# Kernel tuning notes

Hardware: AMD Instinct MI355X
Metric: run time of the kernel (lower is better)

## Reference

```python
import jax, jax.numpy as jnp
import numpy as np
from jax import lax

LB, UB = 0.0, 0.1
N_ITERS = 32  # fixed-point iterations for water-filling rebalance


def _conv(x, w, b):
    y = lax.conv_general_dilated(x, w, (1, 1), ((1, 1), (1, 1)),
                                 dimension_numbers=("NCHW", "OIHW", "NCHW"))
    return y + b[None, :, None, None]


def _maxpool2(x):
    return lax.reduce_window(x, -jnp.inf, lax.max, (1, 1, 2, 2), (1, 1, 2, 2), "VALID")


def _linear(x, w, b):
    return x @ w.T + b


def _gru(x_num, W_ih, W_hh, b_ih, b_hh):
    # x_num: [B, S, N]; torch GRU gate order r, z, n
    B = x_num.shape[0]
    H = W_hh.shape[1]
    xs = jnp.swapaxes(x_num, 0, 1)  # [S, B, N]

    def step(h, x_t):
        gi = x_t @ W_ih.T + b_ih            # [B, 3H]
        gh = h @ W_hh.T + b_hh              # [B, 3H]
        i_r, i_z, i_n = jnp.split(gi, 3, axis=-1)
        h_r, h_z, h_n = jnp.split(gh, 3, axis=-1)
        r = jax.nn.sigmoid(i_r + h_r)
        z = jax.nn.sigmoid(i_z + h_z)
        n = jnp.tanh(i_n + r * h_n)
        h_new = (1.0 - z) * n + z * h
        return h_new, None

    h0 = jnp.zeros((B, H), dtype=x_num.dtype)
    h_last, _ = lax.scan(step, h0, xs)
    return h_last


def _rebalance_one(w):
    # vectorized fixed-point version of the per-sample while-loop water-filling
    def body(carry, _):
        old, wc = carry
        leftover = jnp.sum(old - wc)
        mask = wc != UB
        s = jnp.sum(jnp.where(mask, wc, 0.0))
        gift = jnp.where(mask & (s > 0), leftover * wc / jnp.where(s > 0, s, 1.0), 0.0)
        new_old = wc + gift
        new_wc = jnp.clip(new_old, LB, UB)
        return (new_old, new_wc), None

    init = (w, jnp.clip(w, LB, UB))
    (_, wc), _ = lax.scan(body, init, None, length=N_ITERS)
    return wc


def setup_inputs() -> dict:
    key = jax.random.key(0)
    ks = jax.random.split(key, 16)
    B, S, N, H_IMG, W_IMG, HID = 16, 60, 50, 64, 60, 128
    fc_in = 64 * (H_IMG // 4) * (W_IMG // 4)  # 15360
    sc = 0.05
    return {
        "x_num": jax.random.normal(ks[0], (B, S, N), jnp.float32),
        "x_img": jax.random.uniform(ks[1], (B, N, H_IMG, W_IMG), jnp.float32),
        "conv1_w": jax.random.normal(ks[2], (32, 1, 3, 3), jnp.float32) * sc,
        "conv1_b": jnp.zeros((32,), jnp.float32),
        "conv2_w": jax.random.normal(ks[3], (64, 32, 3, 3), jnp.float32) * sc,
        "conv2_b": jnp.zeros((64,), jnp.float32),
        "fc1_w": jax.random.normal(ks[4], (64, fc_in), jnp.float32) * 0.01,
        "fc1_b": jnp.zeros((64,), jnp.float32),
        "fc_binary_w": jax.random.normal(ks[5], (1, 64), jnp.float32) * sc,
        "fc_binary_b": jnp.zeros((1,), jnp.float32),
        "fc2_w": jax.random.normal(ks[6], (128, 64), jnp.float32) * sc,
        "fc2_b": jnp.zeros((128,), jnp.float32),
        "W_ih": jax.random.normal(ks[7], (3 * HID, N), jnp.float32) * sc,
        "W_hh": jax.random.normal(ks[8], (3 * HID, HID), jnp.float32) * sc,
        "b_ih": jnp.zeros((3 * HID,), jnp.float32),
        "b_hh": jnp.zeros((3 * HID,), jnp.float32),
        "gru_fc_w": jax.random.normal(ks[9], (N, HID), jnp.float32) * sc,
        "gru_fc_b": jnp.zeros((N,), jnp.float32),
        "fusion_w": jax.random.normal(ks[10], (64, N + 128), jnp.float32) * sc,
        "fusion_b": jnp.zeros((64,), jnp.float32),
        "final_w": jax.random.normal(ks[11], (N, 64), jnp.float32) * sc,
        "final_b": jnp.zeros((N,), jnp.float32),
    }


def reference(x_num, x_img, conv1_w, conv1_b, conv2_w, conv2_b, fc1_w, fc1_b,
              fc_binary_w, fc_binary_b, fc2_w, fc2_b, W_ih, W_hh, b_ih, b_hh,
              gru_fc_w, gru_fc_b, fusion_w, fusion_b, final_w, final_b):
    B, S, N = x_num.shape
    # GRU branch: last hidden -> Linear -> [B, N]
    h_last = _gru(x_num, W_ih, W_hh, b_ih, b_hh)
    numerical_features = _linear(h_last, gru_fc_w, gru_fc_b)

    # CNN branch on per-stock chart images
    xi = x_img.reshape(B * N, 1, x_img.shape[2], x_img.shape[3])
    h = _maxpool2(jax.nn.relu(_conv(xi, conv1_w, conv1_b)))
    h = _maxpool2(jax.nn.relu(_conv(h, conv2_w, conv2_b)))
    h = h.reshape(B * N, -1)
    feats = jax.nn.relu(_linear(h, fc1_w, fc1_b))
    binary_pred = jax.nn.sigmoid(_linear(feats, fc_binary_w, fc_binary_b))
    cnn_features = _linear(feats, fc2_w, fc2_b).reshape(B, N, -1).mean(axis=1)

    fused = jax.nn.relu(_linear(jnp.concatenate([numerical_features, cnn_features], axis=1), fusion_w, fusion_b))
    w = jax.nn.softmax(_linear(fused, final_w, final_b), axis=1)
    portfolio_weights = jax.vmap(_rebalance_one)(w)
    return portfolio_weights, binary_pred.reshape(B, N)
```

## Files before the change

kernel.cpp:

```cpp
#include <hip/hip_runtime.h>
#include <hip/hip_bf16.h>

typedef unsigned short ushort_t;
typedef short short8_t __attribute__((ext_vector_type(8)));
typedef float f32x4 __attribute__((ext_vector_type(4)));
typedef float f32x16 __attribute__((ext_vector_type(16)));
typedef ushort_t us4_t __attribute__((ext_vector_type(4)));

#define NBATCH 16
#define SEQ    60
#define NSTK   50
#define HID    128
#define G3     384
#define NIMG   800
#define IH     64
#define IW     60
#define P1H    32
#define P1W    30
#define P2C    64
#define FCIN   15360

#define OFF_WIHT   0u
#define OFF_WHHF   19200u
#define OFF_WPREP  43776u
#define OFF_FC2WT  52992u
#define OFF_WFC1   61184u
#define OFF_GI     552704u
#define OFF_HLAST  921344u
#define OFF_POOL2  923392u
#define OFF_FC1P   7313152u
#define OFF_FC2O   8165120u
#define WS_FLOATS  8267520u

struct __align__(16) ConvS {
    float    imgp[66][62];
    ushort_t pool1t[34][4][34][8];
    ushort_t pool2s[64][240];
    float    w1[288];
    float    b1[32];
};
struct __align__(16) GruS {
    float    gh[16 * 388];
    ushort_t hb[16 * 136];
};
#define SMEM_BYTES 122368
#define ZWORDS ((16368 + 73984) / 4)

__device__ __forceinline__ float fast_sig(float x) {
    const float e = __expf(-x);
    return __builtin_amdgcn_rcpf(1.f + e);
}
__device__ __forceinline__ float fast_tanh(float x) {
    const float xc = fmaxf(fminf(x, 15.f), -15.f);
    const float e = __expf(2.f * xc);
    return (e - 1.f) * __builtin_amdgcn_rcpf(e + 1.f);
}

__global__ __launch_bounds__(256) void k_prep(const float* __restrict__ wih,
                                              const float* __restrict__ whh,
                                              const float* __restrict__ c2w,
                                              const float* __restrict__ fc2w,
                                              const float* __restrict__ fc1w,
                                              float* __restrict__ wihT,
                                              ushort_t* __restrict__ whhf,
                                              ushort_t* __restrict__ wprep,
                                              float* __restrict__ fc2wT,
                                              ushort_t* __restrict__ wfc1)
{
    const int idx = blockIdx.x * 256 + threadIdx.x;
    if (idx < 19200) {
        const int j = idx % G3, k = idx / G3;
        wihT[idx] = wih[j * NSTK + k];
    } else if (idx < 68352) {
        const int e = idx - 19200;
        const int i = e & 7, l = (e >> 3) & 63, ksj = e >> 9;
        const int ks = ksj & 3, jt = ksj >> 2;
        const int j = jt * 16 + (l & 15);
        const int k = ks * 32 + ((l >> 4) << 3) + i;
        __hip_bfloat16 hv = __float2bfloat16(whh[j * HID + k]);
        whhf[e] = *(ushort_t*)&hv;
    } else if (idx < 86784) {
        const int e = idx - 68352;
        const int i = e & 7, l = (e >> 3) & 63, rest = e >> 9;
        const int ks = rest & 1, mt = rest >> 1;
        const int tap = mt % 9, mm = mt / 9;
        const int oc = mm * 32 + (l & 31);
        const int ic = ks * 16 + ((l >> 5) << 3) + i;
        __hip_bfloat16 hv = __float2bfloat16(c2w[((size_t)oc * 32 + ic) * 9 + tap]);
        wprep[e] = *(ushort_t*)&hv;
    } else if (idx < 94976) {
        const int e = idx - 86784;
        const int j = e & 127, k = e >> 7;
        fc2wT[e] = fc2w[j * 64 + k];
    } else if (idx < 1078016) {
        const int e = idx - 94976;
        const int i = e & 7, l = (e >> 3) & 63, rest = e >> 9;
        const int n = rest & 3, T = rest >> 2;
        const int oc = n * 16 + (l & 15);
        const int k = T * 32 + ((l >> 4) << 3) + i;
        __hip_bfloat16 hv = __float2bfloat16(fc1w[(size_t)oc * FCIN + k]);
        wfc1[e] = *(ushort_t*)&hv;
    }
}

__global__ __launch_bounds__(384) void k_gi(const float* __restrict__ xnum,
                                            const float* __restrict__ wihT,
                                            const float* __restrict__ bih,
                                            float* __restrict__ GI)
{
    const int sb = blockIdx.x;
    const int s = sb >> 4, b = sb & 15;
    const int j = threadIdx.x;
    const float* xr = xnum + (size_t)(b * SEQ + s) * NSTK;
    float a = bih[j];
    for (int k = 0; k < NSTK; ++k) a = fmaf(xr[k], wihT[k * G3 + j], a);
    GI[((size_t)s * 16 + b) * G3 + j] = a;
}

__global__ __launch_bounds__(512, 2) void k_mega(const float* __restrict__ x_img,
                                                 const float* __restrict__ c1w,
                                                 const float* __restrict__ c1b,
                                                 const float* __restrict__ c2b,
                                                 const ushort_t* __restrict__ wprep,
                                                 const float* __restrict__ GI,
                                                 const ushort_t* __restrict__ whhf,
                                                 const float* __restrict__ bhh,
                                                 ushort_t* __restrict__ pool2,
                                                 float* __restrict__ hlast)
{
    extern __shared__ char smraw[];
    const int tid = threadIdx.x;
    const int bid = blockIdx.x;

    if (bid == 0) {
        GruS* g = (GruS*)smraw;
        const int w = tid >> 6, l = tid & 63;
        const int arow = l & 15, kq = l >> 4;
        short8_t wfr[3][4];
        #pragma unroll
        for (int jj = 0; jj < 3; ++jj)
            #pragma unroll
            for (int ks = 0; ks < 4; ++ks)
                wfr[jj][ks] = *(const short8_t*)&whhf[((((w * 3 + jj) * 4 + ks) * 64 + l) * 8)];

        const int b = tid >> 5, hh0 = (tid & 31) * 4;
        const f32x4 bhr = *(const f32x4*)&bhh[hh0];
        const f32x4 bhz = *(const f32x4*)&bhh[128 + hh0];
        const f32x4 bhn = *(const f32x4*)&bhh[256 + hh0];
        float h0 = 0.f, h1 = 0.f, h2 = 0.f, h3 = 0.f;
        for (int i = tid; i < 1088; i += 512) ((unsigned int*)g->hb)[i] = 0u;
        const float* gi0 = GI + b * G3 + hh0;
        f32x4 cr = *(const f32x4*)(gi0);
        f32x4 cz = *(const f32x4*)(gi0 + 128);
        f32x4 cn = *(const f32x4*)(gi0 + 256);
        __syncthreads();

        for (int s = 0; s < SEQ; ++s) {
            const int sn = (s + 1 < SEQ) ? s + 1 : s;
            const float* gnx = GI + ((size_t)sn * 16 + b) * G3 + hh0;
            const f32x4 nr = *(const f32x4*)(gnx);
            const f32x4 nz = *(const f32x4*)(gnx + 128);
            const f32x4 nn = *(const f32x4*)(gnx + 256);

            #pragma unroll
            for (int jj = 0; jj < 3; ++jj) {
                f32x4 a = {0.f, 0.f, 0.f, 0.f};
                #pragma unroll
                for (int ks = 0; ks < 4; ++ks) {
                    short8_t af = *(const short8_t*)&g->hb[arow * 136 + ks * 32 + kq * 8];
                    a = __builtin_amdgcn_mfma_f32_16x16x32_bf16(af, wfr[jj][ks], a, 0, 0, 0);
                }
                const int jt = w * 3 + jj;
                #pragma unroll
                for (int r = 0; r < 4; ++r)
                    g->gh[(kq * 4 + r) * 388 + jt * 16 + arow] = a[r];
            }
            __syncthreads();

            const f32x4 gr = *(const f32x4*)&g->gh[b * 388 + hh0];
            const f32x4 gz = *(const f32x4*)&g->gh[b * 388 + 128 + hh0];
            const f32x4 gn = *(const f32x4*)&g->gh[b * 388 + 256 + hh0];
            float hv0, hv1, hv2, hv3;
            {
                const float r0 = fast_sig(cr[0] + gr[0] + bhr[0]);
                const float z0 = fast_sig(cz[0] + gz[0] + bhz[0]);
                const float n0 = fast_tanh(cn[0] + r0 * (gn[0] + bhn[0]));
                hv0 = (1.f - z0) * n0 + z0 * h0;
                const float r1 = fast_sig(cr[1] + gr[1] + bhr[1]);
                const float z1 = fast_sig(cz[1] + gz[1] + bhz[1]);
                const float n1 = fast_tanh(cn[1] + r1 * (gn[1] + bhn[1]));
                hv1 = (1.f - z1) * n1 + z1 * h1;
                const float r2 = fast_sig(cr[2] + gr[2] + bhr[2]);
                const float z2 = fast_sig(cz[2] + gz[2] + bhz[2]);
                const float n2 = fast_tanh(cn[2] + r2 * (gn[2] + bhn[2]));
                hv2 = (1.f - z2) * n2 + z2 * h2;
                const float r3 = fast_sig(cr[3] + gr[3] + bhr[3]);
                const float z3 = fast_sig(cz[3] + gz[3] + bhz[3]);
                const float n3 = fast_tanh(cn[3] + r3 * (gn[3] + bhn[3]));
                hv3 = (1.f - z3) * n3 + z3 * h3;
            }
            h0 = hv0; h1 = hv1; h2 = hv2; h3 = hv3;
            us4_t hp;
            { __hip_bfloat16 t0 = __float2bfloat16(h0); hp[0] = *(ushort_t*)&t0; }
            { __hip_bfloat16 t1 = __float2bfloat16(h1); hp[1] = *(ushort_t*)&t1; }
            { __hip_bfloat16 t2 = __float2bfloat16(h2); hp[2] = *(ushort_t*)&t2; }
            { __hip_bfloat16 t3 = __float2bfloat16(h3); hp[3] = *(ushort_t*)&t3; }
            *(us4_t*)&g->hb[b * 136 + hh0] = hp;
            cr = nr; cz = nz; cn = nn;
            __syncthreads();
        }
        f32x4 ho = {h0, h1, h2, h3};
        *(f32x4*)&hlast[b * HID + hh0] = ho;
        return;
    }

    ConvS* c = (ConvS*)smraw;
    const int img = bid - 1;
    const float* xim = x_img + (size_t)img * (IH * IW);

    for (int i = tid; i < ZWORDS; i += 512) ((unsigned int*)smraw)[i] = 0u;
    __syncthreads();
    for (int i = tid; i < IH * IW; i += 512) {
        const int y = i / IW, x = i - y * IW;
        c->imgp[y + 1][x + 1] = xim[i];
    }
    for (int i = tid; i < 288; i += 512) c->w1[i] = c1w[i];
    if (tid < 32) c->b1[tid] = c1b[tid];
    __syncthreads();

    #pragma unroll
    for (int jj = 0; jj < 8; ++jj) {
        const int j = tid + jj * 512;
        if (j < 3840) {
            const int px = j % 30;
            const int py = (j / 30) & 31;
            const int cg = j / 960;
            float patch[4][4];
            #pragma unroll
            for (int yy = 0; yy < 4; ++yy)
                #pragma unroll
                for (int xx = 0; xx < 4; ++xx)
                    patch[yy][xx] = c->imgp[2 * py + yy][2 * px + xx];
            short8_t outv;
            #pragma unroll
            for (int ch8 = 0; ch8 < 8; ++ch8) {
                const int ch = cg * 8 + ch8;
                float wr[9];
                #pragma unroll
                for (int q = 0; q < 9; ++q) wr[q] = c->w1[ch * 9 + q];
                const float bia = c->b1[ch];
                float best = 0.f;
                #pragma unroll
                for (int dy = 0; dy < 2; ++dy)
                    #pragma unroll
                    for (int dx = 0; dx < 2; ++dx) {
                        float sv = 0.f;
                        #pragma unroll
                        for (int ky = 0; ky < 3; ++ky)
                            #pragma unroll
                            for (int kx = 0; kx < 3; ++kx)
                                sv = fmaf(patch[dy + ky][dx + kx], wr[ky * 3 + kx], sv);
                        best = fmaxf(best, sv + bia);
                    }
                __hip_bfloat16 hv = __float2bfloat16(best);
                outv[ch8] = *(short*)&hv;
            }
            *(short8_t*)&c->pool1t[py + 1][cg][px + 1][0] = outv;
        }
    }
    __syncthreads();

    {
        const int w  = tid >> 6, l = tid & 63;
        const int m  = w & 1;
        const int hi = l >> 5;
        const int col = l & 31;

        short8_t af[9][2];
        #pragma unroll
        for (int tap = 0; tap < 9; ++tap)
            #pragma unroll
            for (int ks = 0; ks < 2; ++ks)
                af[tap][ks] = *(const short8_t*)&wprep[(((m * 9 + tap) * 2 + ks) * 64 + l) * 8];
        float bia[16];
        #pragma unroll
        for (int r = 0; r < 16; ++r)
            bia[r] = c2b[m * 32 + (r & 3) + 8 * (r >> 2) + 4 * hi];

        for (int yp = (w >> 1); yp < 16; yp += 4) {
            const int y0 = 2 * yp;
            f32x16 a0; f32x16 a1;
            #pragma unroll
            for (int r = 0; r < 16; ++r) { a0[r] = 0.f; a1[r] = 0.f; }
            #pragma unroll
            for (int ro = 0; ro < 4; ++ro) {
                short8_t bf[3][2];
                #pragma unroll
                for (int kx = 0; kx < 3; ++kx)
                    #pragma unroll
                    for (int ks = 0; ks < 2; ++ks)
                        bf[kx][ks] = *(const short8_t*)&c->pool1t[y0 + ro][ks * 2 + hi][kx + col][0];
                if (ro < 3) {
                    #pragma unroll
                    for (int kx = 0; kx < 3; ++kx)
                        #pragma unroll
                        for (int ks = 0; ks < 2; ++ks)
                            a0 = __builtin_amdgcn_mfma_f32_32x32x16_bf16(af[ro * 3 + kx][ks], bf[kx][ks], a0, 0, 0, 0);
                }
                if (ro >= 1) {
                    #pragma unroll
                    for (int kx = 0; kx < 3; ++kx)
                        #pragma unroll
                        for (int ks = 0; ks < 2; ++ks)
                            a1 = __builtin_amdgcn_mfma_f32_32x32x16_bf16(af[(ro - 1) * 3 + kx][ks], bf[kx][ks], a1, 0, 0, 0);
                }
            }
            #pragma unroll
            for (int r = 0; r < 16; ++r) {
                float v = fmaxf(a0[r], a1[r]);
                v = fmaxf(v, __shfl_xor(v, 1, 64));
                v = fmaxf(v + bia[r], 0.f);
                if ((col & 1) == 0 && col < 30) {
                    const int oc = m * 32 + (r & 3) + 8 * (r >> 2) + 4 * hi;
                    __hip_bfloat16 hv = __float2bfloat16(v);
                    c->pool2s[oc][yp * 15 + (col >> 1)] = *(ushort_t*)&hv;
                }
            }
        }
    }
    __syncthreads();

    {
        int4* dst = (int4*)(pool2 + (size_t)img * FCIN);
        const int4* src = (const int4*)c->pool2s;
        #pragma unroll
        for (int jj = 0; jj < 4; ++jj) {
            const int i = tid + jj * 512;
            if (i < 1920) dst[i] = src[i];
        }
    }
}

__global__ __launch_bounds__(256) void k_fc1(const ushort_t* __restrict__ pool2,
                                             const ushort_t* __restrict__ wfc1,
                                             float* __restrict__ part)
{
    const int mt = blockIdx.x >> 4;
    const int ks = blockIdx.x & 15;
    const int w = threadIdx.x >> 6, l = threadIdx.x & 63;
    const int arow = l & 15, kq = l >> 4;
    const ushort_t* Ab = pool2 + (size_t)(mt * 64 + w * 16 + arow) * FCIN + ks * 960 + kq * 8;
    const ushort_t* Bb = wfc1 + (size_t)(ks * 120) * 512 + l * 8;
    f32x4 acc0 = {0.f,0.f,0.f,0.f}, acc1 = {0.f,0.f,0.f,0.f};
    f32x4 acc2 = {0.f,0.f,0.f,0.f}, acc3 = {0.f,0.f,0.f,0.f};
    #pragma unroll 6
    for (int t = 0; t < 30; ++t) {
        const short8_t a  = *(const short8_t*)(Ab + t * 32);
        const short8_t b0 = *(const short8_t*)(Bb + (size_t)(t * 4 + 0) * 512);
        const short8_t b1 = *(const short8_t*)(Bb + (size_t)(t * 4 + 1) * 512);
        const short8_t b2 = *(const short8_t*)(Bb + (size_t)(t * 4 + 2) * 512);
        const short8_t b3 = *(const short8_t*)(Bb + (size_t)(t * 4 + 3) * 512);
        acc0 = __builtin_amdgcn_mfma_f32_16x16x32_bf16(a, b0, acc0, 0, 0, 0);
        acc1 = __builtin_amdgcn_mfma_f32_16x16x32_bf16(a, b1, acc1, 0, 0, 0);
        acc2 = __builtin_amdgcn_mfma_f32_16x16x32_bf16(a, b2, acc2, 0, 0, 0);
        acc3 = __builtin_amdgcn_mfma_f32_16x16x32_bf16(a, b3, acc3, 0, 0, 0);
    }
    const int img = mt * 64 + w * 16 + kq * 4;
    #pragma unroll
    for (int r = 0; r < 4; ++r) {
        float* dst = &part[((size_t)ks * 832 + img + r) * 64];
        dst[arow]      = acc0[r];
        dst[16 + arow] = acc1[r];
        dst[32 + arow] = acc2[r];
        dst[48 + arow] = acc3[r];
    }
}

__device__ __forceinline__ float wave_sum(float v) {
    #pragma unroll
    for (int o = 32; o > 0; o >>= 1) v += __shfl_xor(v, o, 64);
    return v;
}
__device__ __forceinline__ float wave_max(float v) {
    #pragma unroll
    for (int o = 32; o > 0; o >>= 1) v = fmaxf(v, __shfl_xor(v, o, 64));
    return v;
}

__global__ __launch_bounds__(64) void k_post(const float* __restrict__ part,
                                             const float* __restrict__ fc1b,
                                             const float* __restrict__ fbw,
                                             const float* __restrict__ fbb,
                                             const float* __restrict__ fc2wT,
                                             const float* __restrict__ fc2b,
                                             float* __restrict__ out,
                                             float* __restrict__ fc2o)
{
    const int img = blockIdx.x, t = threadIdx.x;
    float s = fc1b[t];
    for (int ks = 0; ks < 16; ++ks) s += part[((size_t)ks * 832 + img) * 64 + t];
    const float f = fmaxf(s, 0.f);
    __shared__ float fl[64];
    fl[t] = f;
    __syncthreads();
    const float bsum = wave_sum(f * fbw[t]);
    if (t == 0) out[800 + img] = 1.f / (1.f + expf(-(bsum + fbb[0])));
    float a0 = fc2b[t], a1 = fc2b[t + 64];
    #pragma unroll 8
    for (int k = 0; k < 64; ++k) {
        const float fk = fl[k];
        a0 = fmaf(fk, fc2wT[k * 128 + t], a0);
        a1 = fmaf(fk, fc2wT[k * 128 + 64 + t], a1);
    }
    fc2o[(size_t)img * 128 + t] = a0;
    fc2o[(size_t)img * 128 + 64 + t] = a1;
}

__global__ __launch_bounds__(64) void k_final(const float* __restrict__ hlast,
                                              const float* __restrict__ fc2o,
                                              const float* __restrict__ gw,
                                              const float* __restrict__ gb,
                                              const float* __restrict__ fw,
                                              const float* __restrict__ fb,
                                              const float* __restrict__ finw,
                                              const float* __restrict__ finb,
                                              float* __restrict__ out)
{
    const int b = blockIdx.x, t = threadIdx.x;
    __shared__ float cf[128], nf[64], fu[64];
    #pragma unroll
    for (int jj = 0; jj < 2; ++jj) {
        const int j = t + jj * 64;
        float s = 0.f;
        for (int n = 0; n < NSTK; ++n) s += fc2o[(size_t)(b * NSTK + n) * 128 + j];
        cf[j] = s * (1.0f / 50.0f);
    }
    float s = 0.f;
    if (t < NSTK) {
        s = gb[t];
        for (int k = 0; k < HID; ++k) s = fmaf(hlast[b * HID + k], gw[t * HID + k], s);
    }
    nf[t] = (t < NSTK) ? s : 0.f;
    __syncthreads();
    float f = fb[t];
    for (int k = 0; k < NSTK; ++k) f = fmaf(nf[k], fw[t * 178 + k], f);
    for (int k = 0; k < 128; ++k) f = fmaf(cf[k], fw[t * 178 + 50 + k], f);
    fu[t] = fmaxf(f, 0.f);
    __syncthreads();
    float L = -3.4e38f;
    if (t < NSTK) {
        L = finb[t];
        for (int k = 0; k < 64; ++k) L = fmaf(fu[k], finw[t * 64 + k], L);
    }
    const float m = wave_max(L);
    const float e = (t < NSTK) ? expf(L - m) : 0.f;
    const float se = wave_sum(e);
    const float wv = e / se;
    float old = wv;
    float wc = fminf(fmaxf(wv, 0.f), 0.1f);
    for (int it = 0; it < 32; ++it) {
        const float leftover = wave_sum(old - wc);
        const bool mask = (wc != 0.1f);
        const float ssum = wave_sum(mask ? wc : 0.f);
        const float gift = (mask && ssum > 0.f) ? leftover * wc / ssum : 0.f;
        old = wc + gift;
        wc = fminf(fmaxf(old, 0.f), 0.1f);
    }
    if (t < NSTK) out[b * NSTK + t] = wc;
}

extern "C" void kernel_launch(void* const* d_in, const int* in_sizes, int n_in,
                              void* d_out, int out_size, void* d_ws, size_t ws_size,
                              hipStream_t stream)
{
    const float* x_num = (const float*)d_in[0];
    const float* x_img = (const float*)d_in[1];
    const float* c1w  = (const float*)d_in[2];
    const float* c1b  = (const float*)d_in[3];
    const float* c2w  = (const float*)d_in[4];
    const float* c2b  = (const float*)d_in[5];
    const float* fc1w = (const float*)d_in[6];
    const float* fc1b = (const float*)d_in[7];
    const float* fbw  = (const float*)d_in[8];
    const float* fbb  = (const float*)d_in[9];
    const float* fc2w = (const float*)d_in[10];
    const float* fc2b = (const float*)d_in[11];
    const float* wih  = (const float*)d_in[12];
    const float* whh  = (const float*)d_in[13];
    const float* bih  = (const float*)d_in[14];
    const float* bhh  = (const float*)d_in[15];
    const float* gw   = (const float*)d_in[16];
    const float* gb   = (const float*)d_in[17];
    const float* fw   = (const float*)d_in[18];
    const float* fb   = (const float*)d_in[19];
    const float* finw = (const float*)d_in[20];
    const float* finb = (const float*)d_in[21];
    float* out = (float*)d_out;
    float* ws  = (float*)d_ws;
    if (ws_size < (size_t)WS_FLOATS * 4) return;

    float* wihT     = ws + OFF_WIHT;
    ushort_t* whhf  = (ushort_t*)(ws + OFF_WHHF);
    ushort_t* wprep = (ushort_t*)(ws + OFF_WPREP);
    float* fc2wT    = ws + OFF_FC2WT;
    ushort_t* wfc1  = (ushort_t*)(ws + OFF_WFC1);
    float* GI       = ws + OFF_GI;
    float* hlast    = ws + OFF_HLAST;
    ushort_t* pool2 = (ushort_t*)(ws + OFF_POOL2);
    float* part     = ws + OFF_FC1P;
    float* fc2o     = ws + OFF_FC2O;

    (void)hipFuncSetAttribute(reinterpret_cast<const void*>(k_mega),
                              hipFuncAttributeMaxDynamicSharedMemorySize, SMEM_BYTES);

    k_prep <<<4211, 256, 0, stream>>>(wih, whh, c2w, fc2w, fc1w,
                                      wihT, whhf, wprep, fc2wT, wfc1);
    k_gi   <<<SEQ * NBATCH, 384, 0, stream>>>(x_num, wihT, bih, GI);
    k_mega <<<NIMG + 1, 512, SMEM_BYTES, stream>>>(x_img, c1w, c1b, c2b, wprep,
                                                   GI, whhf, bhh, pool2, hlast);
    k_fc1  <<<13 * 16, 256, 0, stream>>>(pool2, wfc1, part);
    k_post <<<NIMG, 64, 0, stream>>>(part, fc1b, fbw, fbb, fc2wT, fc2b, out, fc2o);
    k_final<<<NBATCH, 64, 0, stream>>>(hlast, fc2o, gw, gb, fw, fb, finw, finb, out);
}
```

Before: 145.0 us.

## Merge prep/GI kernels, shrink conv smem, fuse fc1 with post-processing

Folds the GRU input projection into the weight-prep kernel and drops the wihT/fc2wT transposes. Conv1 now reads weights straight from global memory and handles padding with bounds checks instead of zeroing a padded buffer. Conv2 writes pool2 directly to global memory, and the smaller shared-memory footprint allows raising occupancy to 4 blocks. The split-K fc1 and the separate post kernel are replaced by one kernel doing full-K MFMA per 16 images plus the binary head and fc2. This cuts launches and partial-sum traffic, but fc1 now runs on only 50 blocks with long serial K loops, and the pool2 global stores are scattered.

```diff
diff --git a/kernel.cpp b/kernel.cpp
--- a/kernel.cpp
+++ b/kernel.cpp
@@ -20,31 +20,29 @@
 #define P2C    64
 #define FCIN   15360
 
-#define OFF_WIHT   0u
-#define OFF_WHHF   19200u
-#define OFF_WPREP  43776u
-#define OFF_FC2WT  52992u
-#define OFF_WFC1   61184u
-#define OFF_GI     552704u
-#define OFF_HLAST  921344u
-#define OFF_POOL2  923392u
-#define OFF_FC1P   7313152u
-#define OFF_FC2O   8165120u
-#define WS_FLOATS  8267520u
+#define OFF_WHHF   0u
+#define OFF_WPREP  24576u
+#define OFF_WFC1   33792u
+#define OFF_GI     525312u
+#define OFF_HLAST  893952u
+#define OFF_POOL2  896000u
+#define OFF_FC2O   7040000u
+#define WS_FLOATS  7142400u
+
+#define E_WHH  49152
+#define E_WPR  18432
+#define E_FC1  983040
+#define E_TOT  (E_WHH + E_WPR + E_FC1)
 
 struct __align__(16) ConvS {
-    float    imgp[66][62];
-    ushort_t pool1t[34][4][34][8];
-    ushort_t pool2s[64][240];
-    float    w1[288];
-    float    b1[32];
+    ushort_t pool1t[32][4][32][8];
+    float    imgp[64][60];
 };
 struct __align__(16) GruS {
     float    gh[16 * 388];
     ushort_t hb[16 * 136];
 };
-#define SMEM_BYTES 122368
-#define ZWORDS ((16368 + 73984) / 4)
+#define SMEM_BYTES 80896
 
 __device__ __forceinline__ float fast_sig(float x) {
     const float e = __expf(-x);
@@ -56,31 +54,40 @@
     return (e - 1.f) * __builtin_amdgcn_rcpf(e + 1.f);
 }
 
-__global__ __launch_bounds__(256) void k_prep(const float* __restrict__ wih,
-                                              const float* __restrict__ whh,
-                                              const float* __restrict__ c2w,
-                                              const float* __restrict__ fc2w,
-                                              const float* __restrict__ fc1w,
-                                              float* __restrict__ wihT,
-                                              ushort_t* __restrict__ whhf,
-                                              ushort_t* __restrict__ wprep,
-                                              float* __restrict__ fc2wT,
-                                              ushort_t* __restrict__ wfc1)
+__global__ __launch_bounds__(384) void k_pre(const float* __restrict__ xnum,
+                                             const float* __restrict__ wih,
+                                             const float* __restrict__ bih,
+                                             const float* __restrict__ whh,
+                                             const float* __restrict__ c2w,
+                                             const float* __restrict__ fc1w,
+                                             float* __restrict__ GI,
+                                             ushort_t* __restrict__ whhf,
+                                             ushort_t* __restrict__ wprep,
+                                             ushort_t* __restrict__ wfc1)
 {
-    const int idx = blockIdx.x * 256 + threadIdx.x;
-    if (idx < 19200) {
-        const int j = idx % G3, k = idx / G3;
-        wihT[idx] = wih[j * NSTK + k];
-    } else if (idx < 68352) {
-        const int e = idx - 19200;
+    const int bid = blockIdx.x;
+    if (bid < 960) {
+        const int s = bid >> 4, b = bid & 15;
+        const int j = threadIdx.x;
+        const float* xr = xnum + (size_t)(b * SEQ + s) * NSTK;
+        const float* wr = wih + (size_t)j * NSTK;
+        float a = bih[j];
+        #pragma unroll 10
+        for (int k = 0; k < NSTK; ++k) a = fmaf(xr[k], wr[k], a);
+        GI[((size_t)s * 16 + b) * G3 + j] = a;
+        return;
+    }
+    const int idx = (bid - 960) * 384 + threadIdx.x;
+    if (idx < E_WHH) {
+        const int e = idx;
         const int i = e & 7, l = (e >> 3) & 63, ksj = e >> 9;
         const int ks = ksj & 3, jt = ksj >> 2;
         const int j = jt * 16 + (l & 15);
         const int k = ks * 32 + ((l >> 4) << 3) + i;
         __hip_bfloat16 hv = __float2bfloat16(whh[j * HID + k]);
         whhf[e] = *(ushort_t*)&hv;
-    } else if (idx < 86784) {
-        const int e = idx - 68352;
+    } else if (idx < E_WHH + E_WPR) {
+        const int e = idx - E_WHH;
         const int i = e & 7, l = (e >> 3) & 63, rest = e >> 9;
         const int ks = rest & 1, mt = rest >> 1;
         const int tap = mt % 9, mm = mt / 9;
@@ -88,12 +95,8 @@
         const int ic = ks * 16 + ((l >> 5) << 3) + i;
         __hip_bfloat16 hv = __float2bfloat16(c2w[((size_t)oc * 32 + ic) * 9 + tap]);
         wprep[e] = *(ushort_t*)&hv;
-    } else if (idx < 94976) {
-        const int e = idx - 86784;
-        const int j = e & 127, k = e >> 7;
-        fc2wT[e] = fc2w[j * 64 + k];
-    } else if (idx < 1078016) {
-        const int e = idx - 94976;
+    } else if (idx < E_TOT) {
+        const int e = idx - (E_WHH + E_WPR);
         const int i = e & 7, l = (e >> 3) & 63, rest = e >> 9;
         const int n = rest & 3, T = rest >> 2;
         const int oc = n * 16 + (l & 15);
@@ -103,21 +106,7 @@
     }
 }
 
-__global__ __launch_bounds__(384) void k_gi(const float* __restrict__ xnum,
-                                            const float* __restrict__ wihT,
-                                            const float* __restrict__ bih,
-                                            float* __restrict__ GI)
-{
-    const int sb = blockIdx.x;
-    const int s = sb >> 4, b = sb & 15;
-    const int j = threadIdx.x;
-    const float* xr = xnum + (size_t)(b * SEQ + s) * NSTK;
-    float a = bih[j];
-    for (int k = 0; k < NSTK; ++k) a = fmaf(xr[k], wihT[k * G3 + j], a);
-    GI[((size_t)s * 16 + b) * G3 + j] = a;
-}
-
-__global__ __launch_bounds__(512, 2) void k_mega(const float* __restrict__ x_img,
+__global__ __launch_bounds__(512, 4) void k_mega(const float* __restrict__ x_img,
                                                  const float* __restrict__ c1w,
                                                  const float* __restrict__ c1b,
                                                  const float* __restrict__ c2b,
@@ -218,54 +207,62 @@
     const int img = bid - 1;
     const float* xim = x_img + (size_t)img * (IH * IW);
 
-    for (int i = tid; i < ZWORDS; i += 512) ((unsigned int*)smraw)[i] = 0u;
+    if (tid < 256) {
+        const int y = tid >> 3, cg = (tid >> 1) & 3, xs = (tid & 1) * 31;
+        short8_t z = {0, 0, 0, 0, 0, 0, 0, 0};
+        *(short8_t*)&c->pool1t[y][cg][xs][0] = z;
+    }
+    {
+        const f32x4* src = (const f32x4*)xim;
+        f32x4* dst = (f32x4*)c->imgp;
+        for (int i = tid; i < 3840; i += 512) dst[i] = src[i];
+    }
     __syncthreads();
-    for (int i = tid; i < IH * IW; i += 512) {
-        const int y = i / IW, x = i - y * IW;
-        c->imgp[y + 1][x + 1] = xim[i];
-    }
-    for (int i = tid; i < 288; i += 512) c->w1[i] = c1w[i];
-    if (tid < 32) c->b1[tid] = c1b[tid];
-    __syncthreads();
-
-    #pragma unroll
-    for (int jj = 0; jj < 8; ++jj) {
-        const int j = tid + jj * 512;
-        if (j < 3840) {
-            const int px = j % 30;
-            const int py = (j / 30) & 31;
-            const int cg = j / 960;
+
+    #pragma unroll
+    for (int rep = 0; rep < 2; ++rep) {
+        const int p = tid + rep * 512;
+        if (p < 960) {
+            const int py = p / 30, px = p - py * 30;
             float patch[4][4];
             #pragma unroll
-            for (int yy = 0; yy < 4; ++yy)
+            for (int yy = 0; yy < 4; ++yy) {
+                const int iy = 2 * py - 1 + yy;
                 #pragma unroll
-                for (int xx = 0; xx < 4; ++xx)
-                    patch[yy][xx] = c->imgp[2 * py + yy][2 * px + xx];
-            short8_t outv;
-            #pragma unroll
-            for (int ch8 = 0; ch8 < 8; ++ch8) {
-                const int ch = cg * 8 + ch8;
-                float wr[9];
+                for (int xx = 0; xx < 4; ++xx) {
+                    const int ix = 2 * px - 1 + xx;
+                    patch[yy][xx] = (iy >= 0 && iy < IH && ix >= 0 && ix < IW)
+                                        ? c->imgp[iy][ix] : 0.f;
+                }
+            }
+            #pragma unroll
+            for (int cg = 0; cg < 4; ++cg) {
+                short8_t outv;
                 #pragma unroll
-                for (int q = 0; q < 9; ++q) wr[q] = c->w1[ch * 9 + q];
-                const float bia = c->b1[ch];
-                float best = 0.f;
-                #pragma unroll
-                for (int dy = 0; dy < 2; ++dy)
+                for (int ch8 = 0; ch8 < 8; ++ch8) {
+                    const int ch = cg * 8 + ch8;
+                    float wr[9];
                     #pragma unroll
-                    for (int dx = 0; dx < 2; ++dx) {
-                        float sv = 0.f;
+                    for (int q = 0; q < 9; ++q) wr[q] = c1w[ch * 9 + q];
+                    const float bia = c1b[ch];
+                    float best = 0.f;
+                    #pragma unroll
+                    for (int dy = 0; dy < 2; ++dy)
                         #pragma unroll
-                        for (int ky = 0; ky < 3; ++ky)
+                        for (int dx = 0; dx < 2; ++dx) {
+                            float sv = 0.f;
                             #pragma unroll
-                            for (int kx = 0; kx < 3; ++kx)
-                                sv = fmaf(patch[dy + ky][dx + kx], wr[ky * 3 + kx], sv);
-                        best = fmaxf(best, sv + bia);
-                    }
-                __hip_bfloat16 hv = __float2bfloat16(best);
-                outv[ch8] = *(short*)&hv;
+                            for (int ky = 0; ky < 3; ++ky)
+                                #pragma unroll
+                                for (int kx = 0; kx < 3; ++kx)
+                                    sv = fmaf(patch[dy + ky][dx + kx], wr[ky * 3 + kx], sv);
+                            best = fmaxf(best, sv + bia);
+                        }
+                    __hip_bfloat16 hv = __float2bfloat16(best);
+                    outv[ch8] = *(short*)&hv;
+                }
+                *(short8_t*)&c->pool1t[py][cg][px + 1][0] = outv;
             }
-            *(short8_t*)&c->pool1t[py + 1][cg][px + 1][0] = outv;
         }
     }
     __syncthreads();
@@ -287,19 +284,31 @@
         for (int r = 0; r < 16; ++r)
             bia[r] = c2b[m * 32 + (r & 3) + 8 * (r >> 2) + 4 * hi];
 
+        const bool wr = ((col & 1) == 0) && (col < 30);
+        const int px = col >> 1;
+        ushort_t* p2b = pool2 + (size_t)img * FCIN + px;
+        const short8_t bfz = {0, 0, 0, 0, 0, 0, 0, 0};
+
         for (int yp = (w >> 1); yp < 16; yp += 4) {
-            const int y0 = 2 * yp;
-            f32x16 a0; f32x16 a1;
+            f32x16 a0, a1;
             #pragma unroll
             for (int r = 0; r < 16; ++r) { a0[r] = 0.f; a1[r] = 0.f; }
             #pragma unroll
             for (int ro = 0; ro < 4; ++ro) {
+                const int y = 2 * yp - 1 + ro;
                 short8_t bf[3][2];
-                #pragma unroll
-                for (int kx = 0; kx < 3; ++kx)
+                if (y >= 0 && y < 32) {
                     #pragma unroll
-                    for (int ks = 0; ks < 2; ++ks)
-                        bf[kx][ks] = *(const short8_t*)&c->pool1t[y0 + ro][ks * 2 + hi][kx + col][0];
+                    for (int kx = 0; kx < 3; ++kx)
+                        #pragma unroll
+                        for (int ks = 0; ks < 2; ++ks)
+                            bf[kx][ks] = *(const short8_t*)&c->pool1t[y][ks * 2 + hi][kx + col][0];
+                } else {
+                    #pragma unroll
+                    for (int kx = 0; kx < 3; ++kx)
+                        #pragma unroll
+                        for (int ks = 0; ks < 2; ++ks) bf[kx][ks] = bfz;
+                }
                 if (ro < 3) {
                     #pragma unroll
                     for (int kx = 0; kx < 3; ++kx)
@@ -320,59 +329,68 @@
                 float v = fmaxf(a0[r], a1[r]);
                 v = fmaxf(v, __shfl_xor(v, 1, 64));
                 v = fmaxf(v + bia[r], 0.f);
-                if ((col & 1) == 0 && col < 30) {
+                if (wr) {
                     const int oc = m * 32 + (r & 3) + 8 * (r >> 2) + 4 * hi;
                     __hip_bfloat16 hv = __float2bfloat16(v);
-                    c->pool2s[oc][yp * 15 + (col >> 1)] = *(ushort_t*)&hv;
+                    p2b[oc * 240 + yp * 15] = *(ushort_t*)&hv;
                 }
             }
         }
     }
-    __syncthreads();
-
-    {
-        int4* dst = (int4*)(pool2 + (size_t)img * FCIN);
-        const int4* src = (const int4*)c->pool2s;
-        #pragma unroll
-        for (int jj = 0; jj < 4; ++jj) {
-            const int i = tid + jj * 512;
-            if (i < 1920) dst[i] = src[i];
-        }
-    }
-}
-
-__global__ __launch_bounds__(256) void k_fc1(const ushort_t* __restrict__ pool2,
-                                             const ushort_t* __restrict__ wfc1,
-                                             float* __restrict__ part)
+}
+
+__global__ __launch_bounds__(256) void k_fc1post(const ushort_t* __restrict__ pool2,
+                                                 const ushort_t* __restrict__ wfc1,
+                                                 const float* __restrict__ fc1b,
+                                                 const float* __restrict__ fbw,
+                                                 const float* __restrict__ fbb,
+                                                 const float* __restrict__ fc2w,
+                                                 const float* __restrict__ fc2b,
+                                                 float* __restrict__ out,
+                                                 float* __restrict__ fc2o)
 {
-    const int mt = blockIdx.x >> 4;
-    const int ks = blockIdx.x & 15;
+    const int mt = blockIdx.x;
     const int w = threadIdx.x >> 6, l = threadIdx.x & 63;
     const int arow = l & 15, kq = l >> 4;
-    const ushort_t* Ab = pool2 + (size_t)(mt * 64 + w * 16 + arow) * FCIN + ks * 960 + kq * 8;
-    const ushort_t* Bb = wfc1 + (size_t)(ks * 120) * 512 + l * 8;
-    f32x4 acc0 = {0.f,0.f,0.f,0.f}, acc1 = {0.f,0.f,0.f,0.f};
-    f32x4 acc2 = {0.f,0.f,0.f,0.f}, acc3 = {0.f,0.f,0.f,0.f};
-    #pragma unroll 6
-    for (int t = 0; t < 30; ++t) {
-        const short8_t a  = *(const short8_t*)(Ab + t * 32);
-        const short8_t b0 = *(const short8_t*)(Bb + (size_t)(t * 4 + 0) * 512);
-        const short8_t b1 = *(const short8_t*)(Bb + (size_t)(t * 4 + 1) * 512);
-        const short8_t b2 = *(const short8_t*)(Bb + (size_t)(t * 4 + 2) * 512);
-        const short8_t b3 = *(const short8_t*)(Bb + (size_t)(t * 4 + 3) * 512);
-        acc0 = __builtin_amdgcn_mfma_f32_16x16x32_bf16(a, b0, acc0, 0, 0, 0);
-        acc1 = __builtin_amdgcn_mfma_f32_16x16x32_bf16(a, b1, acc1, 0, 0, 0);
-        acc2 = __builtin_amdgcn_mfma_f32_16x16x32_bf16(a, b2, acc2, 0, 0, 0);
-        acc3 = __builtin_amdgcn_mfma_f32_16x16x32_bf16(a, b3, acc3, 0, 0, 0);
-    }
-    const int img = mt * 64 + w * 16 + kq * 4;
-    #pragma unroll
-    for (int r = 0; r < 4; ++r) {
-        float* dst = &part[((size_t)ks * 832 + img + r) * 64];
-        dst[arow]      = acc0[r];
-        dst[16 + arow] = acc1[r];
-        dst[32 + arow] = acc2[r];
-        dst[48 + arow] = acc3[r];
+    const int img16 = mt * 16;
+    const ushort_t* Ab = pool2 + (size_t)(img16 + arow) * FCIN + kq * 8;
+    const ushort_t* Bb = wfc1 + (size_t)w * 512 + (size_t)l * 8;
+    f32x4 acc0 = {0.f, 0.f, 0.f, 0.f}, acc1 = {0.f, 0.f, 0.f, 0.f};
+    #pragma unroll 4
+    for (int T = 0; T < 480; T += 2) {
+        const short8_t aA = *(const short8_t*)(Ab + (size_t)T * 32);
+        const short8_t bA = *(const short8_t*)(Bb + (size_t)T * 2048);
+        const short8_t aB = *(const short8_t*)(Ab + (size_t)(T + 1) * 32);
+        const short8_t bB = *(const short8_t*)(Bb + (size_t)(T + 1) * 2048);
+        acc0 = __builtin_amdgcn_mfma_f32_16x16x32_bf16(aA, bA, acc0, 0, 0, 0);
+        acc1 = __builtin_amdgcn_mfma_f32_16x16x32_bf16(aB, bB, acc1, 0, 0, 0);
+    }
+    __shared__ float fl[16][64];
+    const int oc = w * 16 + (l & 15);
+    #pragma unroll
+    for (int r = 0; r < 4; ++r)
+        fl[kq * 4 + r][oc] = fmaxf(acc0[r] + acc1[r] + fc1b[oc], 0.f);
+    __syncthreads();
+
+    const int t = threadIdx.x;
+    const int im = t >> 4;
+    float bs = 0.f;
+    #pragma unroll
+    for (int q = 0; q < 4; ++q) {
+        const int k = (t & 15) * 4 + q;
+        bs = fmaf(fl[im][k], fbw[k], bs);
+    }
+    bs += __shfl_xor(bs, 1, 64); bs += __shfl_xor(bs, 2, 64);
+    bs += __shfl_xor(bs, 4, 64); bs += __shfl_xor(bs, 8, 64);
+    if ((t & 15) == 0) out[800 + img16 + im] = 1.f / (1.f + expf(-(bs + fbb[0])));
+
+    #pragma unroll
+    for (int q = 0; q < 8; ++q) {
+        const int j = (t & 15) + q * 16;
+        float a2 = fc2b[j];
+        #pragma unroll 8
+        for (int k = 0; k < 64; ++k) a2 = fmaf(fl[im][k], fc2w[j * 64 + k], a2);
+        fc2o[(size_t)(img16 + im) * 128 + j] = a2;
     }
 }
 
@@ -385,35 +403,6 @@
     #pragma unroll
     for (int o = 32; o > 0; o >>= 1) v = fmaxf(v, __shfl_xor(v, o, 64));
     return v;
-}
-
-__global__ __launch_bounds__(64) void k_post(const float* __restrict__ part,
-                                             const float* __restrict__ fc1b,
-                                             const float* __restrict__ fbw,
-                                             const float* __restrict__ fbb,
-                                             const float* __restrict__ fc2wT,
-                                             const float* __restrict__ fc2b,
-                                             float* __restrict__ out,
-                                             float* __restrict__ fc2o)
-{
-    const int img = blockIdx.x, t = threadIdx.x;
-    float s = fc1b[t];
-    for (int ks = 0; ks < 16; ++ks) s += part[((size_t)ks * 832 + img) * 64 + t];
-    const float f = fmaxf(s, 0.f);
-    __shared__ float fl[64];
-    fl[t] = f;
-    __syncthreads();
-    const float bsum = wave_sum(f * fbw[t]);
-    if (t == 0) out[800 + img] = 1.f / (1.f + expf(-(bsum + fbb[0])));
-    float a0 = fc2b[t], a1 = fc2b[t + 64];
-    #pragma unroll 8
-    for (int k = 0; k < 64; ++k) {
-        const float fk = fl[k];
-        a0 = fmaf(fk, fc2wT[k * 128 + t], a0);
-        a1 = fmaf(fk, fc2wT[k * 128 + 64 + t], a1);
-    }
-    fc2o[(size_t)img * 128 + t] = a0;
-    fc2o[(size_t)img * 128 + 64 + t] = a1;
 }
 
 __global__ __launch_bounds__(64) void k_final(const float* __restrict__ hlast,
@@ -499,26 +488,21 @@
     float* ws  = (float*)d_ws;
     if (ws_size < (size_t)WS_FLOATS * 4) return;
 
-    float* wihT     = ws + OFF_WIHT;
     ushort_t* whhf  = (ushort_t*)(ws + OFF_WHHF);
     ushort_t* wprep = (ushort_t*)(ws + OFF_WPREP);
-    float* fc2wT    = ws + OFF_FC2WT;
     ushort_t* wfc1  = (ushort_t*)(ws + OFF_WFC1);
     float* GI       = ws + OFF_GI;
     float* hlast    = ws + OFF_HLAST;
     ushort_t* pool2 = (ushort_t*)(ws + OFF_POOL2);
-    float* part     = ws + OFF_FC1P;
     float* fc2o     = ws + OFF_FC2O;
 
     (void)hipFuncSetAttribute(reinterpret_cast<const void*>(k_mega),
                               hipFuncAttributeMaxDynamicSharedMemorySize, SMEM_BYTES);
 
-    k_prep <<<4211, 256, 0, stream>>>(wih, whh, c2w, fc2w, fc1w,
-                                      wihT, whhf, wprep, fc2wT, wfc1);
-    k_gi   <<<SEQ * NBATCH, 384, 0, stream>>>(x_num, wihT, bih, GI);
-    k_mega <<<NIMG + 1, 512, SMEM_BYTES, stream>>>(x_img, c1w, c1b, c2b, wprep,
-                                                   GI, whhf, bhh, pool2, hlast);
-    k_fc1  <<<13 * 16, 256, 0, stream>>>(pool2, wfc1, part);
-    k_post <<<NIMG, 64, 0, stream>>>(part, fc1b, fbw, fbb, fc2wT, fc2b, out, fc2o);
-    k_final<<<NBATCH, 64, 0, stream>>>(hlast, fc2o, gw, gb, fw, fb, finw, finb, out);
-}
+    k_pre    <<<960 + 2736, 384, 0, stream>>>(x_num, wih, bih, whh, c2w, fc1w,
+                                              GI, whhf, wprep, wfc1);
+    k_mega   <<<NIMG + 1, 512, SMEM_BYTES, stream>>>(x_img, c1w, c1b, c2b, wprep,
+                                                     GI, whhf, bhh, pool2, hlast);
+    k_fc1post<<<50, 256, 0, stream>>>(pool2, wfc1, fc1b, fbw, fbb, fc2w, fc2b, out, fc2o);
+    k_final  <<<NBATCH, 64, 0, stream>>>(hlast, fc2o, gw, gb, fw, fb, finw, finb, out);
+}
```

Measured after the change: 293.2 us. 2.02x slower.
